# Performance work log

Hardware: AMD Instinct MI355X
Metric: run time of the kernel (lower is better)

Reference implementation:

```python
import jax, jax.numpy as jnp
import numpy as np

B, S, D = 2, 2048, 1024
H, DK, DV = 16, 64, 64


def setup_inputs() -> dict:
    key = jax.random.key(0)
    ks = jax.random.split(key, 11)
    s = 1.0 / np.sqrt(D)
    inp = {
        "Q": jax.random.normal(ks[0], (B, S, D), jnp.float32),
        "K": jax.random.normal(ks[1], (B, S, D), jnp.float32),
        "V": jax.random.normal(ks[2], (B, S, D), jnp.float32),
        "Wq": jax.random.normal(ks[3], (H, D, DK), jnp.float32) * s,
        "bq": jax.random.normal(ks[4], (H, DK), jnp.float32) * 0.01,
        "Wk": jax.random.normal(ks[5], (H, D, DK), jnp.float32) * s,
        "bk": jax.random.normal(ks[6], (H, DK), jnp.float32) * 0.01,
        "Wv": jax.random.normal(ks[7], (H, D, DV), jnp.float32) * s,
        "bv": jax.random.normal(ks[8], (H, DV), jnp.float32) * 0.01,
        "Wm": jax.random.normal(ks[9], (H * DV, D), jnp.float32) * (1.0 / np.sqrt(H * DV)),
        "bm": jax.random.normal(ks[10], (D,), jnp.float32) * 0.01,
    }
    return inp


def reference(Q, K, V, Wq, bq, Wk, bk, Wv, bv, Wm, bm):
    # Per-head projections (batched over heads instead of a Python loop)
    q = jnp.einsum("bqd,hdk->bhqk", Q, Wq) + bq[None, :, None, :]   # [B,H,S,DK]
    k = jnp.einsum("bsd,hdk->bhsk", K, Wk) + bk[None, :, None, :]   # [B,H,S,DK]
    v = jnp.einsum("bsd,hdv->bhsv", V, Wv) + bv[None, :, None, :]   # [B,H,S,DV]
    scores = jnp.einsum("bhqk,bhsk->bhqs", q, k) / jnp.sqrt(jnp.asarray(DK, q.dtype))
    attn = jax.nn.softmax(scores, axis=-1)                           # [B,H,S,S]
    ctx = jnp.einsum("bhqs,bhsv->bhqv", attn, v)                     # [B,H,S,DV]
    # Concat heads along feature dim, then output projection
    stacked_ctx = jnp.transpose(ctx, (0, 2, 1, 3)).reshape(B, S, H * DV)
    multi_head = stacked_ctx @ Wm + bm                               # [B,S,D]
    # torch.cat(attn_weights_list, dim=-1): [B, S, H*S]
    stacked_attention_weights = jnp.transpose(attn, (0, 2, 1, 3)).reshape(B, S, H * S)
    return multi_head, stacked_attention_weights
```

## Files before the change

### kernel.cpp

```cpp
#include <hip/hip_runtime.h>

#define B_ 2
#define S_ 2048
#define D_ 1024
#define H_ 16
#define M_ 4096

typedef unsigned short u16;
typedef unsigned int u32;
typedef short bf8 __attribute__((ext_vector_type(8)));
typedef float f4 __attribute__((ext_vector_type(4)));

#define MFMA16(a, b, c) __builtin_amdgcn_mfma_f32_16x16x32_bf16(a, b, c, 0, 0, 0)

__device__ __forceinline__ u16 f2b(float f) {
  u32 u = __builtin_bit_cast(u32, f);
  u += 0x7fffu + ((u >> 16) & 1);
  return (u16)(u >> 16);
}
__device__ __forceinline__ u32 pack2(float lo, float hi) {
  return (u32)f2b(lo) | ((u32)f2b(hi) << 16);
}
__device__ __forceinline__ float b2f(u16 h) {
  return __builtin_bit_cast(float, (u32)h << 16);
}
__device__ __forceinline__ bf8 g16(const u16* p) { return *(const bf8*)p; }

__device__ __forceinline__ bf8 ldA(const u16* lds, int rowBase, int kc, int lane) {
  int row = rowBase + (lane & 15);
  int c = (kc * 4 + (lane >> 4)) ^ (row & 7);
  return *(const bf8*)(lds + row * 64 + c * 8);
}

__device__ __forceinline__ void stage_async(u16* ldsdst, const u16* __restrict__ gsrc,
                                            int srcStride, int lane) {
  int row = lane >> 3;
  int c16 = (lane & 7) ^ (row & 7);
  const u16* g = gsrc + (size_t)row * srcStride + c16 * 8;
  __builtin_amdgcn_global_load_lds((const __attribute__((address_space(1))) void*)g,
                                   (__attribute__((address_space(3))) void*)ldsdst,
                                   16, 0, 0);
}

__device__ __forceinline__ void stageB(u16* lds, const u16* __restrict__ src,
                                       int srcStride, int t) {
#pragma unroll
  for (int i = 0; i < 4; ++i) {
    int c = t + 256 * i;
    int row = c >> 3, col = c & 7;
    uint4 v = *(const uint4*)(src + (size_t)row * srcStride + col * 8);
    *(uint4*)(lds + row * 64 + (col ^ (row & 7)) * 8) = v;
  }
}

__device__ __forceinline__ void stageAf(u16* lds, const float* __restrict__ src,
                                        int srcStride, int t) {
#pragma unroll
  for (int i = 0; i < 4; ++i) {
    int c = t + 256 * i;
    int row = c >> 3, col = c & 7;
    const float* p = src + (size_t)row * srcStride + col * 8;
    float4 a = *(const float4*)p;
    float4 b = *(const float4*)(p + 4);
    uint4 o;
    o.x = pack2(a.x, a.y);
    o.y = pack2(a.z, a.w);
    o.z = pack2(b.x, b.y);
    o.w = pack2(b.z, b.w);
    *(uint4*)(lds + row * 64 + (col ^ (row & 7)) * 8) = o;
  }
}

__global__ __launch_bounds__(256) void tcvt(const float* __restrict__ in,
                                            u16* __restrict__ out, int R, int C) {
  int rt = blockIdx.x, ct = blockIdx.y, z = blockIdx.z;
  in += (size_t)z * R * C;
  out += (size_t)z * R * C;
  __shared__ float tile[64][65];
  int t = threadIdx.x;
  int r = t >> 2, cc = (t & 3) * 16;
#pragma unroll
  for (int j = 0; j < 16; j += 4) {
    float4 v = *(const float4*)(in + (size_t)(rt * 64 + r) * C + ct * 64 + cc + j);
    tile[r][cc + j] = v.x;
    tile[r][cc + j + 1] = v.y;
    tile[r][cc + j + 2] = v.z;
    tile[r][cc + j + 3] = v.w;
  }
  __syncthreads();
  int c = t >> 2;
  u32 buf[8];
#pragma unroll
  for (int j = 0; j < 8; ++j)
    buf[j] = pack2(tile[cc + 2 * j][c], tile[cc + 2 * j + 1][c]);
  uint4* dst = (uint4*)(out + (size_t)(ct * 64 + c) * R + rt * 64 + cc);
  dst[0] = make_uint4(buf[0], buf[1], buf[2], buf[3]);
  dst[1] = make_uint4(buf[4], buf[5], buf[6], buf[7]);
}

__global__ __launch_bounds__(256) void tb16(const u16* __restrict__ in,
                                            u16* __restrict__ out) {
  int st = blockIdx.x, z = blockIdx.z;
  in += (size_t)z * S_ * 64;
  out += (size_t)z * 64 * S_;
  __shared__ u16 tile[64][72];
  int t = threadIdx.x;
#pragma unroll
  for (int i = 0; i < 2; ++i) {
    int c = t + 256 * i;
    int row = c >> 3, col = (c & 7) * 8;
    uint4 v = *(const uint4*)(in + (size_t)(st * 64 + row) * 64 + col);
    *(uint4*)&tile[row][col] = v;
  }
  __syncthreads();
  int dv = t >> 2, cc = (t & 3) * 16;
  u32 buf[8];
#pragma unroll
  for (int j = 0; j < 8; ++j) {
    u16 a = tile[cc + 2 * j][dv];
    u16 b = tile[cc + 2 * j + 1][dv];
    buf[j] = (u32)a | ((u32)b << 16);
  }
  uint4* dst = (uint4*)(out + (size_t)dv * S_ + st * 64 + cc);
  dst[0] = make_uint4(buf[0], buf[1], buf[2], buf[3]);
  dst[1] = make_uint4(buf[4], buf[5], buf[6], buf[7]);
}

template <int AF32, int SCATTER>
__global__ __launch_bounds__(256) void gemm128(const void* __restrict__ Ap,
                                               const u16* __restrict__ BT,
                                               const float* __restrict__ bias,
                                               void* __restrict__ outp, float scale) {
  int mt = blockIdx.x, nt = blockIdx.y;
  int t = threadIdx.x, lane = t & 63, w = t >> 6;
  int wr = w >> 1, wc = w & 1;
  int quad = lane >> 4, col = lane & 15;
  __shared__ u16 Asm[128 * 64], Bsm[128 * 64];
  f4 acc[4][4] = {};
  for (int kt = 0; kt < 16; ++kt) {
    __syncthreads();
    if (AF32)
      stageAf(Asm, (const float*)Ap + (size_t)(mt * 128) * 1024 + kt * 64, 1024, t);
    else
      stageB(Asm, (const u16*)Ap + (size_t)(mt * 128) * 1024 + kt * 64, 1024, t);
    stageB(Bsm, BT + (size_t)(nt * 128) * 1024 + kt * 64, 1024, t);
    __syncthreads();
#pragma unroll
    for (int kc = 0; kc < 2; ++kc) {
      bf8 a[4], b[4];
#pragma unroll
      for (int fr = 0; fr < 4; ++fr) a[fr] = ldA(Asm, wr * 64 + fr * 16, kc, lane);
#pragma unroll
      for (int nf = 0; nf < 4; ++nf) b[nf] = ldA(Bsm, wc * 64 + nf * 16, kc, lane);
#pragma unroll
      for (int fr = 0; fr < 4; ++fr)
#pragma unroll
        for (int nf = 0; nf < 4; ++nf)
          acc[fr][nf] = MFMA16(a[fr], b[nf], acc[fr][nf]);
    }
  }
#pragma unroll
  for (int fr = 0; fr < 4; ++fr)
#pragma unroll
    for (int nf = 0; nf < 4; ++nf) {
      int n = nt * 128 + wc * 64 + nf * 16 + col;
      float bs = bias[n];
#pragma unroll
      for (int r = 0; r < 4; ++r) {
        int gm = mt * 128 + wr * 64 + fr * 16 + quad * 4 + r;
        if (SCATTER) {
          int h = n >> 6, d = n & 63;
          int bb = gm >> 11, s = gm & 2047;
          ((u16*)outp)[(size_t)((bb * H_ + h) * S_ + s) * 64 + d] =
              f2b((acc[fr][nf][r] + bs) * scale);
        } else {
          ((float*)outp)[(size_t)gm * 1024 + n] = acc[fr][nf][r] + bs;
        }
      }
    }
}

__global__ void attn4(const u16* __restrict__ qp, const u16* __restrict__ kp,
                      const u16* __restrict__ vT, u16* __restrict__ ctxo,
                      float* __restrict__ attw) {
  int bid = blockIdx.x;
  int l = (bid & 7) * 128 + (bid >> 3);
  int qt = l & 31, hb = l >> 5;
  int h = hb & 15, b = hb >> 4;
  int t = threadIdx.x, lane = t & 63, w = t >> 6;
  int quad = lane >> 4, col = lane & 15;

  __shared__ u16 Ksm[2][64 * 64];
  __shared__ u16 Vsm[2][64 * 64];
  __shared__ u16 Psm[4][16 * 64];

  const u16* kbase = kp + (size_t)(b * H_ + h) * S_ * 64;
  const u16* vbase = vT + (size_t)(b * H_ + h) * 64 * S_;
  const u16* qrow = qp + ((size_t)(b * H_ + h) * S_ + qt * 64 + w * 16) * 64;
  int r16 = (lane & 15) * 64;
  int c0 = (lane >> 4) * 8, c1 = c0 + 32;
  bf8 qf0 = g16(qrow + r16 + c0);
  bf8 qf1 = g16(qrow + r16 + c1);

#define SGK(bi, kt)                                                               \
  {                                                                               \
    stage_async(Ksm[bi] + w * 1024, kbase + (size_t)(kt) * 4096 + w * 16 * 64,    \
                64, lane);                                                        \
    stage_async(Ksm[bi] + w * 1024 + 512,                                         \
                kbase + (size_t)(kt) * 4096 + (w * 16 + 8) * 64, 64, lane);       \
  }
#define SGV(bi, kt)                                                               \
  {                                                                               \
    stage_async(Vsm[bi] + w * 1024, vbase + (size_t)(w * 16) * S_ + (kt) * 64,    \
                S_, lane);                                                        \
    stage_async(Vsm[bi] + w * 1024 + 512,                                         \
                vbase + (size_t)(w * 16 + 8) * S_ + (kt) * 64, S_, lane);         \
  }
#define WAITVM(N)                                          \
  asm volatile("s_waitcnt vmcnt(" #N ")" ::: "memory");    \
  __builtin_amdgcn_sched_barrier(0)
#define BAR()                      \
  __builtin_amdgcn_s_barrier();    \
  __builtin_amdgcn_sched_barrier(0)

  SGK(0, 0);
  WAITVM(0);
  BAR();
  float lsum = 0.f;
  for (int kt = 0; kt < 32; ++kt) {
    SGK((kt + 1) & 1, (kt + 1) & 31);
    const u16* Kc = Ksm[kt & 1];
    f4 sc[4] = {};
#pragma unroll
    for (int fr = 0; fr < 4; ++fr) {
      bf8 k0 = ldA(Kc, fr * 16, 0, lane);
      bf8 k1 = ldA(Kc, fr * 16, 1, lane);
      sc[fr] = MFMA16(k0, qf0, sc[fr]);
      sc[fr] = MFMA16(k1, qf1, sc[fr]);
    }
    float s = 0.f;
#pragma unroll
    for (int fr = 0; fr < 4; ++fr)
#pragma unroll
      for (int r = 0; r < 4; ++r) s += __expf(sc[fr][r]);
    lsum += s;
    WAITVM(0);
    BAR();
  }
  lsum += __shfl_xor(lsum, 16);
  lsum += __shfl_xor(lsum, 32);
  float linv = 1.f / lsum;

  SGV(0, 0);
  WAITVM(0);
  BAR();
  f4 ctxa[4] = {};
  u16* Pw = Psm[w];
  size_t awrow = ((size_t)(b * S_ + qt * 64 + w * 16) * H_ + h) * S_;
  for (int kt = 0; kt < 32; ++kt) {
    SGK((kt + 1) & 1, (kt + 1) & 31);
    SGV((kt + 1) & 1, (kt + 1) & 31);
    const u16* Kc = Ksm[kt & 1];
    const u16* Vc = Vsm[kt & 1];
    f4 sc[4] = {};
#pragma unroll
    for (int fr = 0; fr < 4; ++fr) {
      bf8 k0 = ldA(Kc, fr * 16, 0, lane);
      bf8 k1 = ldA(Kc, fr * 16, 1, lane);
      sc[fr] = MFMA16(k0, qf0, sc[fr]);
      sc[fr] = MFMA16(k1, qf1, sc[fr]);
    }
#pragma unroll
    for (int fr = 0; fr < 4; ++fr) {
      float p0 = __expf(sc[fr][0]) * linv;
      float p1 = __expf(sc[fr][1]) * linv;
      float p2 = __expf(sc[fr][2]) * linv;
      float p3 = __expf(sc[fr][3]) * linv;
      int bo = col * 128 + ((fr * 32 + quad * 8) ^ ((col & 7) << 4));
      uint2 u;
      u.x = pack2(p0, p1);
      u.y = pack2(p2, p3);
      *(uint2*)((char*)Pw + bo) = u;
    }
#pragma unroll
    for (int it = 0; it < 2; ++it) {
      int row = (lane >> 3) + 8 * it;
      int cc = lane & 7;
      int bo = row * 128 + ((cc ^ (row & 7)) << 4);
      bf8 pv = *(const bf8*)((const char*)Pw + bo);
      float* dst = attw + awrow + (size_t)row * (H_ * S_) + kt * 64 + cc * 8;
      float4 o0, o1;
      o0.x = b2f((u16)pv[0]);
      o0.y = b2f((u16)pv[1]);
      o0.z = b2f((u16)pv[2]);
      o0.w = b2f((u16)pv[3]);
      o1.x = b2f((u16)pv[4]);
      o1.y = b2f((u16)pv[5]);
      o1.z = b2f((u16)pv[6]);
      o1.w = b2f((u16)pv[7]);
      *(float4*)dst = o0;
      *((float4*)dst + 1) = o1;
    }
    bf8 pf0 = ldA(Pw, 0, 0, lane);
    bf8 pf1 = ldA(Pw, 0, 1, lane);
#pragma unroll
    for (int fr = 0; fr < 4; ++fr) {
      bf8 v0 = ldA(Vc, fr * 16, 0, lane);
      bf8 v1 = ldA(Vc, fr * 16, 1, lane);
      ctxa[fr] = MFMA16(v0, pf0, ctxa[fr]);
      ctxa[fr] = MFMA16(v1, pf1, ctxa[fr]);
    }
    WAITVM(4);
    BAR();
  }
  int qg = qt * 64 + w * 16 + col;
  size_t cb = ((size_t)(b * S_ + qg) * H_ + h) * 64;
#pragma unroll
  for (int fr = 0; fr < 4; ++fr) {
    uint2 u;
    u.x = pack2(ctxa[fr][0], ctxa[fr][1]);
    u.y = pack2(ctxa[fr][2], ctxa[fr][3]);
    *(uint2*)(ctxo + cb + fr * 16 + quad * 4) = u;
  }
#undef SGK
#undef SGV
#undef WAITVM
#undef BAR
}

extern "C" void kernel_launch(void* const* d_in, const int* in_sizes, int n_in,
                              void* d_out, int out_size, void* d_ws, size_t ws_size,
                              hipStream_t stream) {
  const float* Q = (const float*)d_in[0];
  const float* K = (const float*)d_in[1];
  const float* V = (const float*)d_in[2];
  const float* Wq = (const float*)d_in[3];
  const float* bq = (const float*)d_in[4];
  const float* Wk = (const float*)d_in[5];
  const float* bk = (const float*)d_in[6];
  const float* Wv = (const float*)d_in[7];
  const float* bv = (const float*)d_in[8];
  const float* Wm = (const float*)d_in[9];
  const float* bm = (const float*)d_in[10];
  float* out0 = (float*)d_out;
  float* out1 = out0 + (size_t)M_ * D_;
  (void)in_sizes; (void)n_in; (void)out_size; (void)ws_size;

  u16* WT0 = (u16*)d_ws;
  u16* WT1 = WT0 + 1048576;
  u16* WT2 = WT1 + 1048576;
  u16* WT3 = WT2 + 1048576;
  u16* qp = WT3 + 1048576;
  u16* kp = qp + 4194304;
  u16* vp = kp + 4194304;
  u16* vTp = vp + 4194304;

  tcvt<<<dim3(16, 1, 16), 256, 0, stream>>>(Wq, WT0, 1024, 64);
  tcvt<<<dim3(16, 1, 16), 256, 0, stream>>>(Wk, WT1, 1024, 64);
  tcvt<<<dim3(16, 1, 16), 256, 0, stream>>>(Wv, WT2, 1024, 64);
  tcvt<<<dim3(16, 16, 1), 256, 0, stream>>>(Wm, WT3, 1024, 1024);
  gemm128<1, 1><<<dim3(32, 8), 256, 0, stream>>>(Q, WT0, bq, qp, 0.125f);
  gemm128<1, 1><<<dim3(32, 8), 256, 0, stream>>>(K, WT1, bk, kp, 1.0f);
  gemm128<1, 1><<<dim3(32, 8), 256, 0, stream>>>(V, WT2, bv, vp, 1.0f);
  tb16<<<dim3(32, 1, 32), 256, 0, stream>>>(vp, vTp);
  attn4<<<1024, 256, 0, stream>>>(qp, kp, vTp, vp, out1);
  gemm128<0, 0><<<dim3(32, 8), 256, 0, stream>>>(vp, WT3, bm, out0, 1.0f);
}
```

Before: 347.5 us.

## Batch QKV projections into one launch, fuse V transpose, register-load K in pass one

Merges the three Q/K/V weight conversions into one kernel and the three projection GEMMs into one z-batched launch. The V projection now writes its transposed layout directly, which removes the separate transpose kernel and its intermediate buffer. The first attention pass (softmax denominators) loads K straight from global memory into registers with double buffering, dropping the LDS staging and per-tile barriers, and sets launch bounds to allow 4 blocks per CU. This cuts launch overhead and memory traffic, at the cost of more register pressure and strided 8-byte stores for the transposed V.

Result: slower. 374.6 us (+7.8%).

```diff
diff --git a/kernel.cpp b/kernel.cpp
--- a/kernel.cpp
+++ b/kernel.cpp
@@ -98,39 +98,113 @@
   dst[1] = make_uint4(buf[4], buf[5], buf[6], buf[7]);
 }
 
-__global__ __launch_bounds__(256) void tb16(const u16* __restrict__ in,
-                                            u16* __restrict__ out) {
-  int st = blockIdx.x, z = blockIdx.z;
-  in += (size_t)z * S_ * 64;
-  out += (size_t)z * 64 * S_;
-  __shared__ u16 tile[64][72];
+__global__ __launch_bounds__(256) void tcvt3(const float* __restrict__ Wq,
+                                             const float* __restrict__ Wk,
+                                             const float* __restrict__ Wv,
+                                             u16* __restrict__ WT0,
+                                             u16* __restrict__ WT1,
+                                             u16* __restrict__ WT2) {
+  int rt = blockIdx.x, z = blockIdx.z;
+  int mat = z >> 4, hh = z & 15;
+  const float* in = (mat == 0 ? Wq : mat == 1 ? Wk : Wv) + (size_t)hh * 1024 * 64;
+  u16* out = (mat == 0 ? WT0 : mat == 1 ? WT1 : WT2) + (size_t)hh * 1024 * 64;
+  __shared__ float tile[64][65];
   int t = threadIdx.x;
-#pragma unroll
-  for (int i = 0; i < 2; ++i) {
-    int c = t + 256 * i;
-    int row = c >> 3, col = (c & 7) * 8;
-    uint4 v = *(const uint4*)(in + (size_t)(st * 64 + row) * 64 + col);
-    *(uint4*)&tile[row][col] = v;
+  int r = t >> 2, cc = (t & 3) * 16;
+#pragma unroll
+  for (int j = 0; j < 16; j += 4) {
+    float4 v = *(const float4*)(in + (size_t)(rt * 64 + r) * 64 + cc + j);
+    tile[r][cc + j] = v.x;
+    tile[r][cc + j + 1] = v.y;
+    tile[r][cc + j + 2] = v.z;
+    tile[r][cc + j + 3] = v.w;
   }
   __syncthreads();
-  int dv = t >> 2, cc = (t & 3) * 16;
+  int c = t >> 2;
   u32 buf[8];
 #pragma unroll
-  for (int j = 0; j < 8; ++j) {
-    u16 a = tile[cc + 2 * j][dv];
-    u16 b = tile[cc + 2 * j + 1][dv];
-    buf[j] = (u32)a | ((u32)b << 16);
-  }
-  uint4* dst = (uint4*)(out + (size_t)dv * S_ + st * 64 + cc);
+  for (int j = 0; j < 8; ++j)
+    buf[j] = pack2(tile[cc + 2 * j][c], tile[cc + 2 * j + 1][c]);
+  uint4* dst = (uint4*)(out + (size_t)c * 1024 + rt * 64 + cc);
   dst[0] = make_uint4(buf[0], buf[1], buf[2], buf[3]);
   dst[1] = make_uint4(buf[4], buf[5], buf[6], buf[7]);
 }
 
-template <int AF32, int SCATTER>
-__global__ __launch_bounds__(256) void gemm128(const void* __restrict__ Ap,
-                                               const u16* __restrict__ BT,
-                                               const float* __restrict__ bias,
-                                               void* __restrict__ outp, float scale) {
+__global__ __launch_bounds__(256) void proj3(
+    const float* __restrict__ Qf, const float* __restrict__ Kf,
+    const float* __restrict__ Vf, const u16* __restrict__ WT0,
+    const u16* __restrict__ WT1, const u16* __restrict__ WT2,
+    const float* __restrict__ bq, const float* __restrict__ bk,
+    const float* __restrict__ bv, u16* __restrict__ qp, u16* __restrict__ kp,
+    u16* __restrict__ vTp) {
+  int mt = blockIdx.x, nt = blockIdx.y, z = blockIdx.z;
+  const float* Ap = z == 0 ? Qf : z == 1 ? Kf : Vf;
+  const u16* BT = z == 0 ? WT0 : z == 1 ? WT1 : WT2;
+  const float* bias = z == 0 ? bq : z == 1 ? bk : bv;
+  float scale = z == 0 ? 0.125f : 1.0f;
+  int t = threadIdx.x, lane = t & 63, w = t >> 6;
+  int wr = w >> 1, wc = w & 1;
+  int quad = lane >> 4, col = lane & 15;
+  __shared__ u16 Asm[128 * 64], Bsm[128 * 64];
+  f4 acc[4][4] = {};
+  for (int kt = 0; kt < 16; ++kt) {
+    __syncthreads();
+    stageAf(Asm, Ap + (size_t)(mt * 128) * 1024 + kt * 64, 1024, t);
+    stageB(Bsm, BT + (size_t)(nt * 128) * 1024 + kt * 64, 1024, t);
+    __syncthreads();
+#pragma unroll
+    for (int kc = 0; kc < 2; ++kc) {
+      bf8 a[4], b[4];
+#pragma unroll
+      for (int fr = 0; fr < 4; ++fr) a[fr] = ldA(Asm, wr * 64 + fr * 16, kc, lane);
+#pragma unroll
+      for (int nf = 0; nf < 4; ++nf) b[nf] = ldA(Bsm, wc * 64 + nf * 16, kc, lane);
+#pragma unroll
+      for (int fr = 0; fr < 4; ++fr)
+#pragma unroll
+        for (int nf = 0; nf < 4; ++nf)
+          acc[fr][nf] = MFMA16(a[fr], b[nf], acc[fr][nf]);
+    }
+  }
+  if (z < 2) {
+    u16* outp = z == 0 ? qp : kp;
+#pragma unroll
+    for (int fr = 0; fr < 4; ++fr)
+#pragma unroll
+      for (int nf = 0; nf < 4; ++nf) {
+        int n = nt * 128 + wc * 64 + nf * 16 + col;
+        int h = n >> 6, d = n & 63;
+        float bs = bias[n];
+#pragma unroll
+        for (int r = 0; r < 4; ++r) {
+          int gm = mt * 128 + wr * 64 + fr * 16 + quad * 4 + r;
+          int bb = gm >> 11, s = gm & 2047;
+          outp[(size_t)((bb * H_ + h) * S_ + s) * 64 + d] =
+              f2b((acc[fr][nf][r] + bs) * scale);
+        }
+      }
+  } else {
+#pragma unroll
+    for (int fr = 0; fr < 4; ++fr)
+#pragma unroll
+      for (int nf = 0; nf < 4; ++nf) {
+        int n = nt * 128 + wc * 64 + nf * 16 + col;
+        int h = n >> 6, d = n & 63;
+        float bs = bias[n];
+        int s0 = mt * 128 + wr * 64 + fr * 16 + quad * 4;
+        int bb = s0 >> 11, s = s0 & 2047;
+        uint2 u;
+        u.x = pack2(acc[fr][nf][0] + bs, acc[fr][nf][1] + bs);
+        u.y = pack2(acc[fr][nf][2] + bs, acc[fr][nf][3] + bs);
+        *(uint2*)(vTp + (size_t)((bb * H_ + h) * 64 + d) * S_ + s) = u;
+      }
+  }
+}
+
+__global__ __launch_bounds__(256) void gemmo(const u16* __restrict__ A,
+                                             const u16* __restrict__ BT,
+                                             const float* __restrict__ bias,
+                                             float* __restrict__ outp) {
   int mt = blockIdx.x, nt = blockIdx.y;
   int t = threadIdx.x, lane = t & 63, w = t >> 6;
   int wr = w >> 1, wc = w & 1;
@@ -139,10 +213,7 @@
   f4 acc[4][4] = {};
   for (int kt = 0; kt < 16; ++kt) {
     __syncthreads();
-    if (AF32)
-      stageAf(Asm, (const float*)Ap + (size_t)(mt * 128) * 1024 + kt * 64, 1024, t);
-    else
-      stageB(Asm, (const u16*)Ap + (size_t)(mt * 128) * 1024 + kt * 64, 1024, t);
+    stageB(Asm, A + (size_t)(mt * 128) * 1024 + kt * 64, 1024, t);
     stageB(Bsm, BT + (size_t)(nt * 128) * 1024 + kt * 64, 1024, t);
     __syncthreads();
 #pragma unroll
@@ -168,21 +239,16 @@
 #pragma unroll
       for (int r = 0; r < 4; ++r) {
         int gm = mt * 128 + wr * 64 + fr * 16 + quad * 4 + r;
-        if (SCATTER) {
-          int h = n >> 6, d = n & 63;
-          int bb = gm >> 11, s = gm & 2047;
-          ((u16*)outp)[(size_t)((bb * H_ + h) * S_ + s) * 64 + d] =
-              f2b((acc[fr][nf][r] + bs) * scale);
-        } else {
-          ((float*)outp)[(size_t)gm * 1024 + n] = acc[fr][nf][r] + bs;
-        }
+        outp[(size_t)gm * 1024 + n] = acc[fr][nf][r] + bs;
       }
     }
 }
 
-__global__ void attn4(const u16* __restrict__ qp, const u16* __restrict__ kp,
-                      const u16* __restrict__ vT, u16* __restrict__ ctxo,
-                      float* __restrict__ attw) {
+__global__ __launch_bounds__(256, 4) void attn5(const u16* __restrict__ qp,
+                                                const u16* __restrict__ kp,
+                                                const u16* __restrict__ vT,
+                                                u16* __restrict__ ctxo,
+                                                float* __restrict__ attw) {
   int bid = blockIdx.x;
   int l = (bid & 7) * 128 + (bid >> 3);
   int qt = l & 31, hb = l >> 5;
@@ -202,6 +268,43 @@
   bf8 qf0 = g16(qrow + r16 + c0);
   bf8 qf1 = g16(qrow + r16 + c1);
 
+#define LDK(d0, d1, kt)                                    \
+  {                                                        \
+    const u16* kb_ = kbase + (size_t)(kt) * 4096 + r16;    \
+    _Pragma("unroll") for (int fr = 0; fr < 4; ++fr) {     \
+      d0[fr] = g16(kb_ + fr * 1024 + c0);                  \
+      d1[fr] = g16(kb_ + fr * 1024 + c1);                  \
+    }                                                      \
+  }
+#define QKSUM(k0a, k1a)                                    \
+  {                                                        \
+    f4 sc[4] = {};                                         \
+    _Pragma("unroll") for (int fr = 0; fr < 4; ++fr) {     \
+      sc[fr] = MFMA16(k0a[fr], qf0, sc[fr]);               \
+      sc[fr] = MFMA16(k1a[fr], qf1, sc[fr]);               \
+    }                                                      \
+    float s_ = 0.f;                                        \
+    _Pragma("unroll") for (int fr = 0; fr < 4; ++fr)       \
+      _Pragma("unroll") for (int r = 0; r < 4; ++r)        \
+        s_ += __expf(sc[fr][r]);                           \
+    lsum += s_;                                            \
+  }
+
+  float lsum = 0.f;
+  {
+    bf8 ka0[4], ka1[4], kb0[4], kb1[4];
+    LDK(ka0, ka1, 0);
+    for (int kt = 0; kt < 32; kt += 2) {
+      LDK(kb0, kb1, kt + 1);
+      QKSUM(ka0, ka1);
+      if (kt + 2 < 32) LDK(ka0, ka1, kt + 2);
+      QKSUM(kb0, kb1);
+    }
+  }
+  lsum += __shfl_xor(lsum, 16);
+  lsum += __shfl_xor(lsum, 32);
+  float linv = 1.f / lsum;
+
 #define SGK(bi, kt)                                                               \
   {                                                                               \
     stage_async(Ksm[bi] + w * 1024, kbase + (size_t)(kt) * 4096 + w * 16 * 64,    \
@@ -224,33 +327,6 @@
   __builtin_amdgcn_sched_barrier(0)
 
   SGK(0, 0);
-  WAITVM(0);
-  BAR();
-  float lsum = 0.f;
-  for (int kt = 0; kt < 32; ++kt) {
-    SGK((kt + 1) & 1, (kt + 1) & 31);
-    const u16* Kc = Ksm[kt & 1];
-    f4 sc[4] = {};
-#pragma unroll
-    for (int fr = 0; fr < 4; ++fr) {
-      bf8 k0 = ldA(Kc, fr * 16, 0, lane);
-      bf8 k1 = ldA(Kc, fr * 16, 1, lane);
-      sc[fr] = MFMA16(k0, qf0, sc[fr]);
-      sc[fr] = MFMA16(k1, qf1, sc[fr]);
-    }
-    float s = 0.f;
-#pragma unroll
-    for (int fr = 0; fr < 4; ++fr)
-#pragma unroll
-      for (int r = 0; r < 4; ++r) s += __expf(sc[fr][r]);
-    lsum += s;
-    WAITVM(0);
-    BAR();
-  }
-  lsum += __shfl_xor(lsum, 16);
-  lsum += __shfl_xor(lsum, 32);
-  float linv = 1.f / lsum;
-
   SGV(0, 0);
   WAITVM(0);
   BAR();
@@ -322,6 +398,8 @@
     u.y = pack2(ctxa[fr][2], ctxa[fr][3]);
     *(uint2*)(ctxo + cb + fr * 16 + quad * 4) = u;
   }
+#undef LDK
+#undef QKSUM
 #undef SGK
 #undef SGV
 #undef WAITVM
@@ -352,17 +430,13 @@
   u16* WT3 = WT2 + 1048576;
   u16* qp = WT3 + 1048576;
   u16* kp = qp + 4194304;
-  u16* vp = kp + 4194304;
-  u16* vTp = vp + 4194304;
-
-  tcvt<<<dim3(16, 1, 16), 256, 0, stream>>>(Wq, WT0, 1024, 64);
-  tcvt<<<dim3(16, 1, 16), 256, 0, stream>>>(Wk, WT1, 1024, 64);
-  tcvt<<<dim3(16, 1, 16), 256, 0, stream>>>(Wv, WT2, 1024, 64);
+  u16* ctx = kp + 4194304;
+  u16* vTp = ctx + 4194304;
+
+  tcvt3<<<dim3(16, 1, 48), 256, 0, stream>>>(Wq, Wk, Wv, WT0, WT1, WT2);
   tcvt<<<dim3(16, 16, 1), 256, 0, stream>>>(Wm, WT3, 1024, 1024);
-  gemm128<1, 1><<<dim3(32, 8), 256, 0, stream>>>(Q, WT0, bq, qp, 0.125f);
-  gemm128<1, 1><<<dim3(32, 8), 256, 0, stream>>>(K, WT1, bk, kp, 1.0f);
-  gemm128<1, 1><<<dim3(32, 8), 256, 0, stream>>>(V, WT2, bv, vp, 1.0f);
-  tb16<<<dim3(32, 1, 32), 256, 0, stream>>>(vp, vTp);
-  attn4<<<1024, 256, 0, stream>>>(qp, kp, vTp, vp, out1);
-  gemm128<0, 0><<<dim3(32, 8), 256, 0, stream>>>(vp, WT3, bm, out0, 1.0f);
-}
+  proj3<<<dim3(32, 8, 3), 256, 0, stream>>>(Q, K, V, WT0, WT1, WT2, bq, bk, bv,
+                                            qp, kp, vTp);
+  attn5<<<1024, 256, 0, stream>>>(qp, kp, vTp, ctx, out1);
+  gemmo<<<dim3(32, 8), 256, 0, stream>>>(ctx, WT3, bm, out0);
+}
```
